# Kernel tuning notes

Hardware: AMD Instinct MI355X
Metric: run time of the kernel (lower is better)

## Reference

```python
import jax, jax.numpy as jnp
import numpy as np

NEG_SLOPE = 0.01  # nn.LeakyReLU default


def setup_inputs() -> dict:
    key = jax.random.key(0)
    k1, k2, k3, k4, k5, k6 = jax.random.split(key, 6)
    N, E, F_IN, F_OUT = 50000, 800000, 256, 64
    x = jax.random.normal(k1, (N, F_IN), dtype=jnp.float32)
    src = jax.random.randint(k2, (E,), 0, N, dtype=jnp.int32)
    dst = jax.random.randint(k3, (E,), 0, N, dtype=jnp.int32)
    # nn.init.normal_(weight, 0, 0.5) for both Linear layers (no bias)
    W1 = 0.5 * jax.random.normal(k4, (F_OUT, F_IN), dtype=jnp.float32)
    W2 = 0.5 * jax.random.normal(k5, (F_OUT, F_OUT), dtype=jnp.float32)
    # detGAT.a = torch.rand(2*out_feats, 1)
    a = jax.random.uniform(k6, (2 * F_OUT, 1), dtype=jnp.float32)
    return {"x": x, "W1": W1, "W2": W2, "a": a, "src": src, "dst": dst}


def reference(x, W1, W2, a, src, dst):
    N, d = x.shape[0], W1.shape[0]
    # model_base: linear -> (dropout, identity in eval) -> relu, twice
    z = jax.nn.relu(x @ W1.T)
    h = jax.nn.relu(z @ W2.T)  # [N, d]
    # detGAT edge score: LeakyReLU(concat([h_dst, h_src]) @ a)
    # split a so we compute per-node dot products once instead of an [E, 2d] concat
    a_dst, a_src = a[:d, 0], a[d:, 0]
    s_dst = h @ a_dst  # [N]
    s_src = h @ a_src  # [N]
    score = jax.nn.leaky_relu(s_dst[dst] + s_src[src], NEG_SLOPE)  # [E]
    # edge_softmax: softmax over incoming edges of each destination node
    m = jax.ops.segment_max(score, dst, num_segments=N)  # [N]
    e = jnp.exp(score - m[dst])
    ssum = jax.ops.segment_sum(e, dst, num_segments=N)  # [N]
    w = e / ssum[dst]  # [E]
    # weighted scatter-sum of src features to dst nodes
    res = jax.ops.segment_sum(h[src] * w[:, None], dst, num_segments=N)  # [N, d]
    return jax.nn.relu(h - res)
```

## Files before the change

### kernel.cpp

```cpp
#include <hip/hip_runtime.h>
#include <math.h>

#define F_IN 256
#define F_OUT 64
#define NEG_SLOPE 0.01f
#define CAP 8192
#define SB 64

typedef unsigned short ushort8_t __attribute__((ext_vector_type(8)));
typedef __bf16 bf16x8 __attribute__((ext_vector_type(8)));
typedef float f32x16 __attribute__((ext_vector_type(16)));

__device__ inline unsigned short f2bf(float f) {
    unsigned u = __float_as_uint(f);
    u += 0x7FFF + ((u >> 16) & 1);
    return (unsigned short)(u >> 16);
}
__device__ inline float bf2f(unsigned short u) {
    return __uint_as_float(((unsigned)u) << 16);
}
__device__ inline void splitbf(float x, unsigned short& hi, unsigned short& lo) {
    hi = f2bf(x);
    lo = f2bf(x - bf2f(hi));
}
__device__ inline bf16x8 asbf8(ushort8_t u) {
    union { ushort8_t u; bf16x8 b; } c; c.u = u; return c.b;
}
__device__ inline float redq32(float v) {
    v += __shfl_xor(v, 1);  v += __shfl_xor(v, 2);  v += __shfl_xor(v, 4);
    v += __shfl_xor(v, 8);  v += __shfl_xor(v, 16);
    return v;
}

__global__ __launch_bounds__(256)
void prep_kernel(const float* __restrict__ W1, const float* __restrict__ W2,
                 unsigned short* __restrict__ w1fh, unsigned short* __restrict__ w1fl,
                 unsigned short* __restrict__ w2fh, unsigned short* __restrict__ w2fl,
                 int* __restrict__ cursor)
{
    int idx = blockIdx.x * 256 + threadIdx.x;
    if (blockIdx.x == 0) cursor[threadIdx.x] = 0;
    int jj = idx & 7, l = (idx >> 3) & 63, t = idx >> 9;
    {
        int nt = t & 1, gks = t >> 1;
        int f = nt * 32 + (l & 31);
        int k = gks * 16 + (l >> 5) * 8 + jj;
        unsigned short hi, lo;
        splitbf(W1[f * F_IN + k], hi, lo);
        w1fh[idx] = hi; w1fl[idx] = lo;
    }
    if (idx < 4096) {
        int nt = t & 1, ks = t >> 1;
        int f = nt * 32 + (l & 31);
        int j = ks * 16 + (l >> 5) * 8 + jj;
        unsigned short hi, lo;
        splitbf(W2[f * F_OUT + j], hi, lo);
        w2fh[idx] = hi; w2fl[idx] = lo;
    }
}

__global__ __launch_bounds__(256, 2)
void mlp_scatter_kernel(const float* __restrict__ x,
                        const unsigned short* __restrict__ w1fh,
                        const unsigned short* __restrict__ w1fl,
                        const unsigned short* __restrict__ w2fh,
                        const unsigned short* __restrict__ w2fl,
                        const float* __restrict__ a,
                        unsigned short* __restrict__ hb,
                        float* __restrict__ sdst,
                        float* __restrict__ ssrc, int N,
                        const int* __restrict__ src, const int* __restrict__ dst,
                        int* __restrict__ cursor, int* __restrict__ edata,
                        int E, int chunk, int MLPB)
{
    __shared__ __align__(16) unsigned short zbuf[4 * 8576];

    const int tid = threadIdx.x;
    const int lane = tid & 63;
    const int bid = blockIdx.x;

    if (bid < MLPB) {
        const int wid = __builtin_amdgcn_readfirstlane(tid >> 6);
        const int ml = lane & 31;
        const int q = lane >> 5;
        const int hl = lane >> 5;
        const int cl = lane & 31;
        const int node0w = bid * 128 + wid * 32;

        unsigned short* xh = zbuf + wid * 8576;
        unsigned short* xl = xh + 4288;
        unsigned short* zh = xh;
        unsigned short* zl = xh + 2112;

        f32x16 acc0, acc1;
#pragma unroll
        for (int i = 0; i < 16; i++) { acc0[i] = 0.f; acc1[i] = 0.f; }

#pragma unroll
        for (int half = 0; half < 2; half++) {
            float4 v[16];
#pragma unroll
            for (int i = 0; i < 16; i++) {
                int r = 2 * i + hl;
                int rr = min(node0w + r, N - 1);
                v[i] = *(const float4*)(x + (size_t)rr * F_IN + half * 128 + cl * 4);
            }
#pragma unroll
            for (int i = 0; i < 16; i++) {
                int r = 2 * i + hl;
                ushort4 h4, l4;
                unsigned short th, tl;
                splitbf(v[i].x, th, tl); h4.x = th; l4.x = tl;
                splitbf(v[i].y, th, tl); h4.y = th; l4.y = tl;
                splitbf(v[i].z, th, tl); h4.z = th; l4.z = tl;
                splitbf(v[i].w, th, tl); h4.w = th; l4.w = tl;
                *(ushort4*)(xh + r * 134 + cl * 4) = h4;
                *(ushort4*)(xl + r * 134 + cl * 4) = l4;
            }
#pragma unroll
            for (int ks = 0; ks < 8; ks++) {
                int gks = half * 8 + ks;
                bf16x8 ah = asbf8(*(const ushort8_t*)(xh + ml * 134 + ks * 16 + q * 8));
                bf16x8 al = asbf8(*(const ushort8_t*)(xl + ml * 134 + ks * 16 + q * 8));
                bf16x8 bh0 = asbf8(*(const ushort8_t*)(w1fh + ((gks * 2 + 0) * 64 + lane) * 8));
                bf16x8 bl0 = asbf8(*(const ushort8_t*)(w1fl + ((gks * 2 + 0) * 64 + lane) * 8));
                bf16x8 bh1 = asbf8(*(const ushort8_t*)(w1fh + ((gks * 2 + 1) * 64 + lane) * 8));
                bf16x8 bl1 = asbf8(*(const ushort8_t*)(w1fl + ((gks * 2 + 1) * 64 + lane) * 8));
                acc0 = __builtin_amdgcn_mfma_f32_32x32x16_bf16(ah, bh0, acc0, 0, 0, 0);
                acc0 = __builtin_amdgcn_mfma_f32_32x32x16_bf16(ah, bl0, acc0, 0, 0, 0);
                acc0 = __builtin_amdgcn_mfma_f32_32x32x16_bf16(al, bh0, acc0, 0, 0, 0);
                acc1 = __builtin_amdgcn_mfma_f32_32x32x16_bf16(ah, bh1, acc1, 0, 0, 0);
                acc1 = __builtin_amdgcn_mfma_f32_32x32x16_bf16(ah, bl1, acc1, 0, 0, 0);
                acc1 = __builtin_amdgcn_mfma_f32_32x32x16_bf16(al, bh1, acc1, 0, 0, 0);
            }
        }

#pragma unroll
        for (int reg = 0; reg < 16; reg++) {
            int nd = (reg & 3) + 8 * (reg >> 2) + 4 * q;
            float z0 = fmaxf(acc0[reg], 0.f);
            float z1 = fmaxf(acc1[reg], 0.f);
            unsigned short h_, l_;
            splitbf(z0, h_, l_);
            zh[nd * 66 + ml] = h_; zl[nd * 66 + ml] = l_;
            splitbf(z1, h_, l_);
            zh[nd * 66 + 32 + ml] = h_; zl[nd * 66 + 32 + ml] = l_;
        }

        f32x16 hacc0, hacc1;
#pragma unroll
        for (int i = 0; i < 16; i++) { hacc0[i] = 0.f; hacc1[i] = 0.f; }
#pragma unroll
        for (int ks = 0; ks < 4; ks++) {
            bf16x8 wh0 = asbf8(*(const ushort8_t*)(w2fh + ((ks * 2 + 0) * 64 + lane) * 8));
            bf16x8 wl0 = asbf8(*(const ushort8_t*)(w2fl + ((ks * 2 + 0) * 64 + lane) * 8));
            bf16x8 wh1 = asbf8(*(const ushort8_t*)(w2fh + ((ks * 2 + 1) * 64 + lane) * 8));
            bf16x8 wl1 = asbf8(*(const ushort8_t*)(w2fl + ((ks * 2 + 1) * 64 + lane) * 8));
            bf16x8 ah = asbf8(*(const ushort8_t*)(zh + ml * 66 + ks * 16 + q * 8));
            bf16x8 al = asbf8(*(const ushort8_t*)(zl + ml * 66 + ks * 16 + q * 8));
            hacc0 = __builtin_amdgcn_mfma_f32_32x32x16_bf16(ah, wh0, hacc0, 0, 0, 0);
            hacc0 = __builtin_amdgcn_mfma_f32_32x32x16_bf16(ah, wl0, hacc0, 0, 0, 0);
            hacc0 = __builtin_amdgcn_mfma_f32_32x32x16_bf16(al, wh0, hacc0, 0, 0, 0);
            hacc1 = __builtin_amdgcn_mfma_f32_32x32x16_bf16(ah, wh1, hacc1, 0, 0, 0);
            hacc1 = __builtin_amdgcn_mfma_f32_32x32x16_bf16(ah, wl1, hacc1, 0, 0, 0);
            hacc1 = __builtin_amdgcn_mfma_f32_32x32x16_bf16(al, wh1, hacc1, 0, 0, 0);
        }

        const float aD0 = a[ml],            aD1 = a[32 + ml];
        const float aS0 = a[F_OUT + ml],    aS1 = a[F_OUT + 32 + ml];

        float sdv = 0.f, ssv = 0.f;
#pragma unroll
        for (int reg = 0; reg < 16; reg++) {
            int nd = (reg & 3) + 8 * (reg >> 2) + 4 * q;
            float h0 = fmaxf(hacc0[reg], 0.f);
            float h1 = fmaxf(hacc1[reg], 0.f);
            float td = redq32(h0 * aD0 + h1 * aD1);
            float ts = redq32(h0 * aS0 + h1 * aS1);
            if (ml == nd) { sdv = td; ssv = ts; }
            int gn = node0w + nd;
            if (gn < N) {
                hb[(size_t)gn * F_OUT + ml]      = f2bf(h0);
                hb[(size_t)gn * F_OUT + 32 + ml] = f2bf(h1);
            }
        }
        {
            int gn = node0w + ml;
            if ((((ml >> 2) & 1) == q) && gn < N) {
                sdst[gn] = sdv;
                ssrc[gn] = ssv;
            }
        }
        return;
    }

    const int sbid = bid - MLPB;
    int* lh = (int*)zbuf;
    int* lbase = lh + 256;
    int* lcur = lh + 512;
    lh[tid] = 0;
    __syncthreads();
    const int beg = sbid * chunk;
    const int end = min(E, beg + chunk);
    for (int i = beg + tid; i < end; i += 256)
        atomicAdd(&lh[((unsigned)dst[i]) >> 8], 1);
    __syncthreads();
    {
        int c = lh[tid];
        lbase[tid] = c ? atomicAdd(&cursor[tid], c) : 0;
        lcur[tid] = 0;
    }
    __syncthreads();
    for (int i = beg + tid; i < end; i += 256) {
        int d = dst[i];
        int s = src[i];
        int b = ((unsigned)d) >> 8;
        int rk = atomicAdd(&lcur[b], 1);
        edata[b * CAP + lbase[b] + rk] = ((d & 0xFF) << 16) | s;
    }
}

__global__ __launch_bounds__(1024)
void sortagg_kernel(const int* __restrict__ cursor,
                    const int* __restrict__ edata,
                    const unsigned short* __restrict__ hb,
                    const float* __restrict__ sdst,
                    const float* __restrict__ ssrc,
                    float* __restrict__ out, int N)
{
    __shared__ int hist[256];
    __shared__ int excl[256];
    __shared__ int start_s[256];
    __shared__ unsigned short ssl[CAP];
    __shared__ float2 ws_sh[16][64];

    const int tid = threadIdx.x;
    const int lane = tid & 63;
    const int wid = tid >> 6;
    const int cb = blockIdx.x;
    const int base = cb * CAP;
    const int ecnt = cursor[cb];

    if (tid < 256) hist[tid] = 0;
    __syncthreads();
    for (int i = tid; i < ecnt; i += 1024)
        atomicAdd(&hist[((unsigned)edata[base + i]) >> 16], 1);
    __syncthreads();

    if (tid < 64) {
        int v0 = hist[lane * 4], v1 = hist[lane * 4 + 1];
        int v2 = hist[lane * 4 + 2], v3 = hist[lane * 4 + 3];
        int ts = v0 + v1 + v2 + v3;
        int s = ts;
#pragma unroll
        for (int d = 1; d < 64; d <<= 1) {
            int t = __shfl_up(s, d);
            if (lane >= d) s += t;
        }
        int e = s - ts;
        excl[lane * 4] = e;
        excl[lane * 4 + 1] = e + v0;
        excl[lane * 4 + 2] = e + v0 + v1;
        excl[lane * 4 + 3] = e + v0 + v1 + v2;
    }
    __syncthreads();
    if (tid < 256) start_s[tid] = excl[tid];
    __syncthreads();

    for (int i = tid; i < ecnt; i += 1024) {
        int pack = edata[base + i];
        int low = ((unsigned)pack) >> 16;
        int rk = atomicAdd(&excl[low], 1);
        ssl[rk] = (unsigned short)(pack & 0xFFFF);
    }
    __syncthreads();

    const int g = lane >> 4;
    const int li = lane & 15;
    const int grp = wid * 4 + g;

    for (int rep = 0; rep < 4; rep++) {
        const int local = rep * 64 + grp;
        const int d = cb * 256 + local;
        const bool vd = d < N;
        const int off = vd ? start_s[local] : 0;
        const int deg = vd ? hist[local] : 0;
        const float sdd = vd ? sdst[d] : 0.f;

        float M = -INFINITY, S = 0.f;
        float c0 = 0.f, c1 = 0.f, c2 = 0.f, c3 = 0.f;

        for (int ch = 0; ch < deg; ch += 16) {
            int ce = min(16, deg - ch);
            float score = -INFINITY;
            int s = 0;
            if (li < ce) {
                s = ssl[off + ch + li];
                float sc = sdd + ssrc[s];
                score = sc > 0.f ? sc : NEG_SLOPE * sc;
            }
            float mc = score;
            mc = fmaxf(mc, __shfl_xor(mc, 1));
            mc = fmaxf(mc, __shfl_xor(mc, 2));
            mc = fmaxf(mc, __shfl_xor(mc, 4));
            mc = fmaxf(mc, __shfl_xor(mc, 8));
            float newM = fmaxf(M, mc);
            float scale = __expf(M - newM);
            float w = (li < ce) ? __expf(score - newM) : 0.f;
            ws_sh[wid][lane] = make_float2(w, __int_as_float(s));
            float csum = w;
            csum += __shfl_xor(csum, 1);
            csum += __shfl_xor(csum, 2);
            csum += __shfl_xor(csum, 4);
            csum += __shfl_xor(csum, 8);
            S = S * scale + csum;
            __builtin_amdgcn_wave_barrier();

            float t0 = 0.f, t1 = 0.f, t2 = 0.f, t3 = 0.f;
#pragma unroll
            for (int e = 0; e < 16; e++) {
                float2 tw = ws_sh[wid][g * 16 + e];
                int se = __float_as_int(tw.y);
                ushort4 r = *(const ushort4*)(hb + (((size_t)(unsigned)se) << 6) + li * 4);
                t0 = fmaf(tw.x, bf2f(r.x), t0);
                t1 = fmaf(tw.x, bf2f(r.y), t1);
                t2 = fmaf(tw.x, bf2f(r.z), t2);
                t3 = fmaf(tw.x, bf2f(r.w), t3);
            }
            c0 = c0 * scale + t0;
            c1 = c1 * scale + t1;
            c2 = c2 * scale + t2;
            c3 = c3 * scale + t3;
            __builtin_amdgcn_wave_barrier();
            M = newM;
        }

        if (vd) {
            ushort4 hr = *(const ushort4*)(hb + (((size_t)(unsigned)d) << 6) + li * 4);
            float inv = (S > 0.f) ? 1.f / S : 0.f;
            float r0 = bf2f(hr.x) - c0 * inv;
            float r1 = bf2f(hr.y) - c1 * inv;
            float r2 = bf2f(hr.z) - c2 * inv;
            float r3 = bf2f(hr.w) - c3 * inv;
            float4 o;
            o.x = r0 > 0.f ? r0 : 0.f;
            o.y = r1 > 0.f ? r1 : 0.f;
            o.z = r2 > 0.f ? r2 : 0.f;
            o.w = r3 > 0.f ? r3 : 0.f;
            *(float4*)(out + (size_t)d * F_OUT + li * 4) = o;
        }
    }
}

extern "C" void kernel_launch(void* const* d_in, const int* in_sizes, int n_in,
                              void* d_out, int out_size, void* d_ws,
                              size_t ws_size, hipStream_t stream)
{
    const float* x  = (const float*)d_in[0];
    const float* W1 = (const float*)d_in[1];
    const float* W2 = (const float*)d_in[2];
    const float* a  = (const float*)d_in[3];
    const int* src  = (const int*)d_in[4];
    const int* dst  = (const int*)d_in[5];
    const int N = in_sizes[0] / F_IN;
    const int E = in_sizes[4];

    float* ws = (float*)d_ws;
    float* sdst = ws;
    float* ssrc = sdst + N;
    unsigned short* w1fh = (unsigned short*)(ssrc + N);
    unsigned short* w1fl = w1fh + 16384;
    unsigned short* w2fh = w1fl + 16384;
    unsigned short* w2fl = w2fh + 4096;
    unsigned short* hb = w2fl + 4096;
    int* cursor = (int*)(hb + (size_t)N * F_OUT);
    int* edata  = cursor + 256;

    const int nbc = (N + 255) >> 8;
    const int MLPB = (N + 127) >> 7;
    const int chunk = (E + SB - 1) / SB;

    prep_kernel<<<64, 256, 0, stream>>>(W1, W2, w1fh, w1fl, w2fh, w2fl, cursor);
    mlp_scatter_kernel<<<MLPB + SB, 256, 0, stream>>>(x, w1fh, w1fl, w2fh, w2fl, a,
                                                      hb, sdst, ssrc, N,
                                                      src, dst, cursor, edata,
                                                      E, chunk, MLPB);
    sortagg_kernel<<<nbc, 1024, 0, stream>>>(cursor, edata, hb, sdst, ssrc,
                                             (float*)d_out, N);
}
```

Before: 147.9 us.

## Software-pipeline x loads in quarter chunks and halve LDS for higher occupancy

Splits the K dimension of the first GEMM into four 64-wide quarters instead of two halves, prefetching the next quarter of x into registers while the current one is split to bf16 and fed to MFMA. This halves the per-wave LDS staging buffer and raises launch bounds from 2 to 4 blocks per SM, aiming to hide global load latency and improve occupancy. The register prefetch plus a tighter register budget may cause spills, and the last iteration issues a redundant reload of quarter 3. The zl region (offset 2112, size up to 2112) still fits within the 4480-element per-wave slot.

Result: slower. 150.8 us (+2.0%).

```diff
diff --git a/kernel.cpp b/kernel.cpp
--- a/kernel.cpp
+++ b/kernel.cpp
@@ -59,7 +59,7 @@
     }
 }
 
-__global__ __launch_bounds__(256, 2)
+__global__ __launch_bounds__(256, 4)
 void mlp_scatter_kernel(const float* __restrict__ x,
                         const unsigned short* __restrict__ w1fh,
                         const unsigned short* __restrict__ w1fl,
@@ -73,7 +73,7 @@
                         int* __restrict__ cursor, int* __restrict__ edata,
                         int E, int chunk, int MLPB)
 {
-    __shared__ __align__(16) unsigned short zbuf[4 * 8576];
+    __shared__ __align__(16) unsigned short zbuf[4 * 4480];
 
     const int tid = threadIdx.x;
     const int lane = tid & 63;
@@ -83,12 +83,12 @@
         const int wid = __builtin_amdgcn_readfirstlane(tid >> 6);
         const int ml = lane & 31;
         const int q = lane >> 5;
-        const int hl = lane >> 5;
-        const int cl = lane & 31;
+        const int rq = lane >> 4;
+        const int cq = lane & 15;
         const int node0w = bid * 128 + wid * 32;
 
-        unsigned short* xh = zbuf + wid * 8576;
-        unsigned short* xl = xh + 4288;
+        unsigned short* xh = zbuf + wid * 4480;
+        unsigned short* xl = xh + 2240;
         unsigned short* zh = xh;
         unsigned short* zl = xh + 2112;
 
@@ -96,32 +96,41 @@
 #pragma unroll
         for (int i = 0; i < 16; i++) { acc0[i] = 0.f; acc1[i] = 0.f; }
 
-#pragma unroll
-        for (int half = 0; half < 2; half++) {
-            float4 v[16];
-#pragma unroll
-            for (int i = 0; i < 16; i++) {
-                int r = 2 * i + hl;
-                int rr = min(node0w + r, N - 1);
-                v[i] = *(const float4*)(x + (size_t)rr * F_IN + half * 128 + cl * 4);
-            }
-#pragma unroll
-            for (int i = 0; i < 16; i++) {
-                int r = 2 * i + hl;
+        int srow[8];
+#pragma unroll
+        for (int i = 0; i < 8; i++)
+            srow[i] = min(node0w + i * 4 + rq, N - 1);
+
+        float4 v[8];
+#pragma unroll
+        for (int i = 0; i < 8; i++)
+            v[i] = *(const float4*)(x + (size_t)srow[i] * F_IN + cq * 4);
+
+#pragma unroll
+        for (int qt = 0; qt < 4; qt++) {
+            const int nqt = qt < 3 ? qt + 1 : 3;
+            float4 vn[8];
+#pragma unroll
+            for (int i = 0; i < 8; i++)
+                vn[i] = *(const float4*)(x + (size_t)srow[i] * F_IN + nqt * 64 + cq * 4);
+
+#pragma unroll
+            for (int i = 0; i < 8; i++) {
+                int r = i * 4 + rq;
                 ushort4 h4, l4;
                 unsigned short th, tl;
                 splitbf(v[i].x, th, tl); h4.x = th; l4.x = tl;
                 splitbf(v[i].y, th, tl); h4.y = th; l4.y = tl;
                 splitbf(v[i].z, th, tl); h4.z = th; l4.z = tl;
                 splitbf(v[i].w, th, tl); h4.w = th; l4.w = tl;
-                *(ushort4*)(xh + r * 134 + cl * 4) = h4;
-                *(ushort4*)(xl + r * 134 + cl * 4) = l4;
-            }
-#pragma unroll
-            for (int ks = 0; ks < 8; ks++) {
-                int gks = half * 8 + ks;
-                bf16x8 ah = asbf8(*(const ushort8_t*)(xh + ml * 134 + ks * 16 + q * 8));
-                bf16x8 al = asbf8(*(const ushort8_t*)(xl + ml * 134 + ks * 16 + q * 8));
+                *(ushort4*)(xh + r * 70 + cq * 4) = h4;
+                *(ushort4*)(xl + r * 70 + cq * 4) = l4;
+            }
+#pragma unroll
+            for (int ks = 0; ks < 4; ks++) {
+                int gks = qt * 4 + ks;
+                bf16x8 ah = asbf8(*(const ushort8_t*)(xh + ml * 70 + ks * 16 + q * 8));
+                bf16x8 al = asbf8(*(const ushort8_t*)(xl + ml * 70 + ks * 16 + q * 8));
                 bf16x8 bh0 = asbf8(*(const ushort8_t*)(w1fh + ((gks * 2 + 0) * 64 + lane) * 8));
                 bf16x8 bl0 = asbf8(*(const ushort8_t*)(w1fl + ((gks * 2 + 0) * 64 + lane) * 8));
                 bf16x8 bh1 = asbf8(*(const ushort8_t*)(w1fh + ((gks * 2 + 1) * 64 + lane) * 8));
@@ -133,6 +142,8 @@
                 acc1 = __builtin_amdgcn_mfma_f32_32x32x16_bf16(ah, bl1, acc1, 0, 0, 0);
                 acc1 = __builtin_amdgcn_mfma_f32_32x32x16_bf16(al, bh1, acc1, 0, 0, 0);
             }
+#pragma unroll
+            for (int i = 0; i < 8; i++) v[i] = vn[i];
         }
 
 #pragma unroll
```

## Stream x tiles via global_load_lds double-buffer and split to bf16 in registers

Applied to the files above, without the earlier changes.

Replaces the load-all-rows-then-convert-to-LDS staging of x with a direct global-to-LDS async copy (global_load_lds) into two per-wave fp32 buffers. These are double-buffered across 8 K-stages with vmcnt waits, and the buffer index is XOR-swizzled to avoid bank conflicts. The hi/lo bf16 split now happens in registers right before the MFMAs, and the smaller LDS footprint allows occupancy to rise to 4 blocks per CU. The intent is to overlap x loads with matrix work and cut register and LDS pressure. The risks are manual vmcnt accounting correctness and redundant split work.

New measurement: 151.4 us. 2.4% more time.

```diff
diff --git a/kernel.cpp b/kernel.cpp
--- a/kernel.cpp
+++ b/kernel.cpp
@@ -26,10 +26,30 @@
 __device__ inline bf16x8 asbf8(ushort8_t u) {
     union { ushort8_t u; bf16x8 b; } c; c.u = u; return c.b;
 }
+__device__ inline void split8(const float4& p0, const float4& p1, bf16x8& ah, bf16x8& al) {
+    ushort8_t h, l;
+    unsigned short th, tl;
+    splitbf(p0.x, th, tl); h[0] = th; l[0] = tl;
+    splitbf(p0.y, th, tl); h[1] = th; l[1] = tl;
+    splitbf(p0.z, th, tl); h[2] = th; l[2] = tl;
+    splitbf(p0.w, th, tl); h[3] = th; l[3] = tl;
+    splitbf(p1.x, th, tl); h[4] = th; l[4] = tl;
+    splitbf(p1.y, th, tl); h[5] = th; l[5] = tl;
+    splitbf(p1.z, th, tl); h[6] = th; l[6] = tl;
+    splitbf(p1.w, th, tl); h[7] = th; l[7] = tl;
+    ah = asbf8(h); al = asbf8(l);
+}
 __device__ inline float redq32(float v) {
     v += __shfl_xor(v, 1);  v += __shfl_xor(v, 2);  v += __shfl_xor(v, 4);
     v += __shfl_xor(v, 8);  v += __shfl_xor(v, 16);
     return v;
+}
+
+__device__ inline void gll16(const void* gsrc, void* lds) {
+    __builtin_amdgcn_global_load_lds(
+        (const __attribute__((address_space(1))) unsigned int*)gsrc,
+        (__attribute__((address_space(3))) unsigned int*)lds,
+        16, 0, 0);
 }
 
 __global__ __launch_bounds__(256)
@@ -59,7 +79,7 @@
     }
 }
 
-__global__ __launch_bounds__(256, 2)
+__global__ __launch_bounds__(256, 4)
 void mlp_scatter_kernel(const float* __restrict__ x,
                         const unsigned short* __restrict__ w1fh,
                         const unsigned short* __restrict__ w1fl,
@@ -73,7 +93,7 @@
                         int* __restrict__ cursor, int* __restrict__ edata,
                         int E, int chunk, int MLPB)
 {
-    __shared__ __align__(16) unsigned short zbuf[4 * 8576];
+    __shared__ __align__(16) unsigned short zbuf[4 * 4224];
 
     const int tid = threadIdx.x;
     const int lane = tid & 63;
@@ -83,45 +103,57 @@
         const int wid = __builtin_amdgcn_readfirstlane(tid >> 6);
         const int ml = lane & 31;
         const int q = lane >> 5;
-        const int hl = lane >> 5;
-        const int cl = lane & 31;
         const int node0w = bid * 128 + wid * 32;
 
-        unsigned short* xh = zbuf + wid * 8576;
-        unsigned short* xl = xh + 4288;
-        unsigned short* zh = xh;
-        unsigned short* zl = xh + 2112;
+        float* bufA = (float*)(zbuf + wid * 4224);
+        float* bufB = (float*)(zbuf + wid * 4224 + 2112);
+        unsigned short* zh = zbuf + wid * 4224;
+        unsigned short* zl = zh + 2112;
+
+        const int rrel_base = lane >> 3;
+        const int slot_w = (lane & 7) >> 1;
+        const int half_w = lane & 1;
 
         f32x16 acc0, acc1;
 #pragma unroll
         for (int i = 0; i < 16; i++) { acc0[i] = 0.f; acc1[i] = 0.f; }
 
-#pragma unroll
-        for (int half = 0; half < 2; half++) {
-            float4 v[16];
-#pragma unroll
-            for (int i = 0; i < 16; i++) {
-                int r = 2 * i + hl;
-                int rr = min(node0w + r, N - 1);
-                v[i] = *(const float4*)(x + (size_t)rr * F_IN + half * 128 + cl * 4);
-            }
-#pragma unroll
-            for (int i = 0; i < 16; i++) {
-                int r = 2 * i + hl;
-                ushort4 h4, l4;
-                unsigned short th, tl;
-                splitbf(v[i].x, th, tl); h4.x = th; l4.x = tl;
-                splitbf(v[i].y, th, tl); h4.y = th; l4.y = tl;
-                splitbf(v[i].z, th, tl); h4.z = th; l4.z = tl;
-                splitbf(v[i].w, th, tl); h4.w = th; l4.w = tl;
-                *(ushort4*)(xh + r * 134 + cl * 4) = h4;
-                *(ushort4*)(xl + r * 134 + cl * 4) = l4;
-            }
-#pragma unroll
-            for (int ks = 0; ks < 8; ks++) {
-                int gks = half * 8 + ks;
-                bf16x8 ah = asbf8(*(const ushort8_t*)(xh + ml * 134 + ks * 16 + q * 8));
-                bf16x8 al = asbf8(*(const ushort8_t*)(xl + ml * 134 + ks * 16 + q * 8));
+        {
+#pragma unroll
+            for (int i = 0; i < 4; i++) {
+                int rrel = i * 8 + rrel_base;
+                int r = min(node0w + rrel, N - 1);
+                int gblk = slot_w ^ (rrel & 3);
+                gll16(x + (size_t)r * F_IN + 0 * 32 + gblk * 8 + half_w * 4,
+                      (char*)bufA + i * 1024);
+            }
+        }
+#pragma unroll
+        for (int st = 0; st < 8; st++) {
+            float* cur = (st & 1) ? bufB : bufA;
+            float* nxt = (st & 1) ? bufA : bufB;
+            if (st < 7) {
+#pragma unroll
+                for (int i = 0; i < 4; i++) {
+                    int rrel = i * 8 + rrel_base;
+                    int r = min(node0w + rrel, N - 1);
+                    int gblk = slot_w ^ (rrel & 3);
+                    gll16(x + (size_t)r * F_IN + (st + 1) * 32 + gblk * 8 + half_w * 4,
+                          (char*)nxt + i * 1024);
+                }
+                asm volatile("s_waitcnt vmcnt(4)" ::: "memory");
+            } else {
+                asm volatile("s_waitcnt vmcnt(0)" ::: "memory");
+            }
+#pragma unroll
+            for (int ks = 0; ks < 2; ks++) {
+                int gks = st * 2 + ks;
+                int sl = (ks * 2 + q) ^ (ml & 3);
+                const float* p = cur + ml * 32 + sl * 8;
+                float4 lo = *(const float4*)p;
+                float4 hi = *(const float4*)(p + 4);
+                bf16x8 ah, al;
+                split8(lo, hi, ah, al);
                 bf16x8 bh0 = asbf8(*(const ushort8_t*)(w1fh + ((gks * 2 + 0) * 64 + lane) * 8));
                 bf16x8 bl0 = asbf8(*(const ushort8_t*)(w1fl + ((gks * 2 + 0) * 64 + lane) * 8));
                 bf16x8 bh1 = asbf8(*(const ushort8_t*)(w1fh + ((gks * 2 + 1) * 64 + lane) * 8));
```

## Move edge scatter into prep kernel with 1024-thread blocks, split MLP kernel

Applied to the files above, without the earlier changes.

The edge bucket-scatter pass leaves the MLP kernel and now runs inside the weight-prep kernel, using 256 blocks of 1024 threads instead of 64 blocks of 256. The MLP runs as its own kernel, and the cursor reset becomes a hipMemsetAsync. The aim is to spread the scatter over more of the GPU and make the MLP kernel simpler. In exchange there is an extra launch plus a memset, and the scatter no longer runs alongside the MLP blocks.

New measurement: 152.8 us. 3.3% more time.

```diff
diff --git a/kernel.cpp b/kernel.cpp
--- a/kernel.cpp
+++ b/kernel.cpp
@@ -5,7 +5,7 @@
 #define F_OUT 64
 #define NEG_SLOPE 0.01f
 #define CAP 8192
-#define SB 64
+#define NB2 256
 
 typedef unsigned short ushort8_t __attribute__((ext_vector_type(8)));
 typedef __bf16 bf16x8 __attribute__((ext_vector_type(8)));
@@ -32,191 +32,187 @@
     return v;
 }
 
-__global__ __launch_bounds__(256)
-void prep_kernel(const float* __restrict__ W1, const float* __restrict__ W2,
-                 unsigned short* __restrict__ w1fh, unsigned short* __restrict__ w1fl,
-                 unsigned short* __restrict__ w2fh, unsigned short* __restrict__ w2fl,
-                 int* __restrict__ cursor)
+__global__ __launch_bounds__(1024)
+void prep_scatter_kernel(const float* __restrict__ W1, const float* __restrict__ W2,
+                         unsigned short* __restrict__ w1fh, unsigned short* __restrict__ w1fl,
+                         unsigned short* __restrict__ w2fh, unsigned short* __restrict__ w2fl,
+                         const int* __restrict__ src, const int* __restrict__ dst,
+                         int* __restrict__ cursor, int* __restrict__ edata,
+                         int E, int chunk)
 {
-    int idx = blockIdx.x * 256 + threadIdx.x;
-    if (blockIdx.x == 0) cursor[threadIdx.x] = 0;
-    int jj = idx & 7, l = (idx >> 3) & 63, t = idx >> 9;
-    {
-        int nt = t & 1, gks = t >> 1;
-        int f = nt * 32 + (l & 31);
-        int k = gks * 16 + (l >> 5) * 8 + jj;
-        unsigned short hi, lo;
-        splitbf(W1[f * F_IN + k], hi, lo);
-        w1fh[idx] = hi; w1fl[idx] = lo;
-    }
-    if (idx < 4096) {
-        int nt = t & 1, ks = t >> 1;
-        int f = nt * 32 + (l & 31);
-        int j = ks * 16 + (l >> 5) * 8 + jj;
-        unsigned short hi, lo;
-        splitbf(W2[f * F_OUT + j], hi, lo);
-        w2fh[idx] = hi; w2fl[idx] = lo;
-    }
-}
-
-__global__ __launch_bounds__(256, 2)
-void mlp_scatter_kernel(const float* __restrict__ x,
-                        const unsigned short* __restrict__ w1fh,
-                        const unsigned short* __restrict__ w1fl,
-                        const unsigned short* __restrict__ w2fh,
-                        const unsigned short* __restrict__ w2fl,
-                        const float* __restrict__ a,
-                        unsigned short* __restrict__ hb,
-                        float* __restrict__ sdst,
-                        float* __restrict__ ssrc, int N,
-                        const int* __restrict__ src, const int* __restrict__ dst,
-                        int* __restrict__ cursor, int* __restrict__ edata,
-                        int E, int chunk, int MLPB)
-{
-    __shared__ __align__(16) unsigned short zbuf[4 * 8576];
-
+    __shared__ int lh[256], lbase[256], lcur[256];
     const int tid = threadIdx.x;
-    const int lane = tid & 63;
-    const int bid = blockIdx.x;
-
-    if (bid < MLPB) {
-        const int wid = __builtin_amdgcn_readfirstlane(tid >> 6);
-        const int ml = lane & 31;
-        const int q = lane >> 5;
-        const int hl = lane >> 5;
-        const int cl = lane & 31;
-        const int node0w = bid * 128 + wid * 32;
-
-        unsigned short* xh = zbuf + wid * 8576;
-        unsigned short* xl = xh + 4288;
-        unsigned short* zh = xh;
-        unsigned short* zl = xh + 2112;
-
-        f32x16 acc0, acc1;
-#pragma unroll
-        for (int i = 0; i < 16; i++) { acc0[i] = 0.f; acc1[i] = 0.f; }
-
-#pragma unroll
-        for (int half = 0; half < 2; half++) {
-            float4 v[16];
-#pragma unroll
-            for (int i = 0; i < 16; i++) {
-                int r = 2 * i + hl;
-                int rr = min(node0w + r, N - 1);
-                v[i] = *(const float4*)(x + (size_t)rr * F_IN + half * 128 + cl * 4);
-            }
-#pragma unroll
-            for (int i = 0; i < 16; i++) {
-                int r = 2 * i + hl;
-                ushort4 h4, l4;
-                unsigned short th, tl;
-                splitbf(v[i].x, th, tl); h4.x = th; l4.x = tl;
-                splitbf(v[i].y, th, tl); h4.y = th; l4.y = tl;
-                splitbf(v[i].z, th, tl); h4.z = th; l4.z = tl;
-                splitbf(v[i].w, th, tl); h4.w = th; l4.w = tl;
-                *(ushort4*)(xh + r * 134 + cl * 4) = h4;
-                *(ushort4*)(xl + r * 134 + cl * 4) = l4;
-            }
-#pragma unroll
-            for (int ks = 0; ks < 8; ks++) {
-                int gks = half * 8 + ks;
-                bf16x8 ah = asbf8(*(const ushort8_t*)(xh + ml * 134 + ks * 16 + q * 8));
-                bf16x8 al = asbf8(*(const ushort8_t*)(xl + ml * 134 + ks * 16 + q * 8));
-                bf16x8 bh0 = asbf8(*(const ushort8_t*)(w1fh + ((gks * 2 + 0) * 64 + lane) * 8));
-                bf16x8 bl0 = asbf8(*(const ushort8_t*)(w1fl + ((gks * 2 + 0) * 64 + lane) * 8));
-                bf16x8 bh1 = asbf8(*(const ushort8_t*)(w1fh + ((gks * 2 + 1) * 64 + lane) * 8));
-                bf16x8 bl1 = asbf8(*(const ushort8_t*)(w1fl + ((gks * 2 + 1) * 64 + lane) * 8));
-                acc0 = __builtin_amdgcn_mfma_f32_32x32x16_bf16(ah, bh0, acc0, 0, 0, 0);
-                acc0 = __builtin_amdgcn_mfma_f32_32x32x16_bf16(ah, bl0, acc0, 0, 0, 0);
-                acc0 = __builtin_amdgcn_mfma_f32_32x32x16_bf16(al, bh0, acc0, 0, 0, 0);
-                acc1 = __builtin_amdgcn_mfma_f32_32x32x16_bf16(ah, bh1, acc1, 0, 0, 0);
-                acc1 = __builtin_amdgcn_mfma_f32_32x32x16_bf16(ah, bl1, acc1, 0, 0, 0);
-                acc1 = __builtin_amdgcn_mfma_f32_32x32x16_bf16(al, bh1, acc1, 0, 0, 0);
-            }
-        }
-
-#pragma unroll
-        for (int reg = 0; reg < 16; reg++) {
-            int nd = (reg & 3) + 8 * (reg >> 2) + 4 * q;
-            float z0 = fmaxf(acc0[reg], 0.f);
-            float z1 = fmaxf(acc1[reg], 0.f);
-            unsigned short h_, l_;
-            splitbf(z0, h_, l_);
-            zh[nd * 66 + ml] = h_; zl[nd * 66 + ml] = l_;
-            splitbf(z1, h_, l_);
-            zh[nd * 66 + 32 + ml] = h_; zl[nd * 66 + 32 + ml] = l_;
-        }
-
-        f32x16 hacc0, hacc1;
-#pragma unroll
-        for (int i = 0; i < 16; i++) { hacc0[i] = 0.f; hacc1[i] = 0.f; }
-#pragma unroll
-        for (int ks = 0; ks < 4; ks++) {
-            bf16x8 wh0 = asbf8(*(const ushort8_t*)(w2fh + ((ks * 2 + 0) * 64 + lane) * 8));
-            bf16x8 wl0 = asbf8(*(const ushort8_t*)(w2fl + ((ks * 2 + 0) * 64 + lane) * 8));
-            bf16x8 wh1 = asbf8(*(const ushort8_t*)(w2fh + ((ks * 2 + 1) * 64 + lane) * 8));
-            bf16x8 wl1 = asbf8(*(const ushort8_t*)(w2fl + ((ks * 2 + 1) * 64 + lane) * 8));
-            bf16x8 ah = asbf8(*(const ushort8_t*)(zh + ml * 66 + ks * 16 + q * 8));
-            bf16x8 al = asbf8(*(const ushort8_t*)(zl + ml * 66 + ks * 16 + q * 8));
-            hacc0 = __builtin_amdgcn_mfma_f32_32x32x16_bf16(ah, wh0, hacc0, 0, 0, 0);
-            hacc0 = __builtin_amdgcn_mfma_f32_32x32x16_bf16(ah, wl0, hacc0, 0, 0, 0);
-            hacc0 = __builtin_amdgcn_mfma_f32_32x32x16_bf16(al, wh0, hacc0, 0, 0, 0);
-            hacc1 = __builtin_amdgcn_mfma_f32_32x32x16_bf16(ah, wh1, hacc1, 0, 0, 0);
-            hacc1 = __builtin_amdgcn_mfma_f32_32x32x16_bf16(ah, wl1, hacc1, 0, 0, 0);
-            hacc1 = __builtin_amdgcn_mfma_f32_32x32x16_bf16(al, wh1, hacc1, 0, 0, 0);
-        }
-
-        const float aD0 = a[ml],            aD1 = a[32 + ml];
-        const float aS0 = a[F_OUT + ml],    aS1 = a[F_OUT + 32 + ml];
-
-        float sdv = 0.f, ssv = 0.f;
-#pragma unroll
-        for (int reg = 0; reg < 16; reg++) {
-            int nd = (reg & 3) + 8 * (reg >> 2) + 4 * q;
-            float h0 = fmaxf(hacc0[reg], 0.f);
-            float h1 = fmaxf(hacc1[reg], 0.f);
-            float td = redq32(h0 * aD0 + h1 * aD1);
-            float ts = redq32(h0 * aS0 + h1 * aS1);
-            if (ml == nd) { sdv = td; ssv = ts; }
-            int gn = node0w + nd;
-            if (gn < N) {
-                hb[(size_t)gn * F_OUT + ml]      = f2bf(h0);
-                hb[(size_t)gn * F_OUT + 32 + ml] = f2bf(h1);
-            }
-        }
+
+    if (blockIdx.x < 16) {
+        int idx = blockIdx.x * 1024 + tid;
+        int jj = idx & 7, l = (idx >> 3) & 63, t = idx >> 9;
         {
-            int gn = node0w + ml;
-            if ((((ml >> 2) & 1) == q) && gn < N) {
-                sdst[gn] = sdv;
-                ssrc[gn] = ssv;
-            }
+            int nt = t & 1, gks = t >> 1;
+            int f = nt * 32 + (l & 31);
+            int k = gks * 16 + (l >> 5) * 8 + jj;
+            unsigned short hi, lo;
+            splitbf(W1[f * F_IN + k], hi, lo);
+            w1fh[idx] = hi; w1fl[idx] = lo;
+        }
+        if (idx < 4096) {
+            int nt = t & 1, ks = t >> 1;
+            int f = nt * 32 + (l & 31);
+            int j = ks * 16 + (l >> 5) * 8 + jj;
+            unsigned short hi, lo;
+            splitbf(W2[f * F_OUT + j], hi, lo);
+            w2fh[idx] = hi; w2fl[idx] = lo;
         }
         return;
     }
 
-    const int sbid = bid - MLPB;
-    int* lh = (int*)zbuf;
-    int* lbase = lh + 256;
-    int* lcur = lh + 512;
-    lh[tid] = 0;
-    __syncthreads();
-    const int beg = sbid * chunk;
+    const int bid = blockIdx.x - 16;
+    if (tid < 256) lh[tid] = 0;
+    __syncthreads();
+    const int beg = bid * chunk;
     const int end = min(E, beg + chunk);
-    for (int i = beg + tid; i < end; i += 256)
+    for (int i = beg + tid; i < end; i += 1024)
         atomicAdd(&lh[((unsigned)dst[i]) >> 8], 1);
     __syncthreads();
-    {
+    if (tid < 256) {
         int c = lh[tid];
         lbase[tid] = c ? atomicAdd(&cursor[tid], c) : 0;
         lcur[tid] = 0;
     }
     __syncthreads();
-    for (int i = beg + tid; i < end; i += 256) {
+    for (int i = beg + tid; i < end; i += 1024) {
         int d = dst[i];
         int s = src[i];
         int b = ((unsigned)d) >> 8;
         int rk = atomicAdd(&lcur[b], 1);
         edata[b * CAP + lbase[b] + rk] = ((d & 0xFF) << 16) | s;
+    }
+}
+
+__global__ __launch_bounds__(256, 2)
+void mlp_kernel(const float* __restrict__ x,
+                const unsigned short* __restrict__ w1fh,
+                const unsigned short* __restrict__ w1fl,
+                const unsigned short* __restrict__ w2fh,
+                const unsigned short* __restrict__ w2fl,
+                const float* __restrict__ a,
+                unsigned short* __restrict__ hb,
+                float* __restrict__ sdst,
+                float* __restrict__ ssrc, int N)
+{
+    __shared__ __align__(16) unsigned short zbuf[4 * 8576];
+
+    const int tid = threadIdx.x;
+    const int lane = tid & 63;
+    const int wid = __builtin_amdgcn_readfirstlane(tid >> 6);
+    const int ml = lane & 31;
+    const int q = lane >> 5;
+    const int hl = lane >> 5;
+    const int cl = lane & 31;
+    const int node0w = blockIdx.x * 128 + wid * 32;
+
+    unsigned short* xh = zbuf + wid * 8576;
+    unsigned short* xl = xh + 4288;
+    unsigned short* zh = xh;
+    unsigned short* zl = xh + 2112;
+
+    f32x16 acc0, acc1;
+#pragma unroll
+    for (int i = 0; i < 16; i++) { acc0[i] = 0.f; acc1[i] = 0.f; }
+
+#pragma unroll
+    for (int half = 0; half < 2; half++) {
+        float4 v[16];
+#pragma unroll
+        for (int i = 0; i < 16; i++) {
+            int r = 2 * i + hl;
+            int rr = min(node0w + r, N - 1);
+            v[i] = *(const float4*)(x + (size_t)rr * F_IN + half * 128 + cl * 4);
+        }
+#pragma unroll
+        for (int i = 0; i < 16; i++) {
+            int r = 2 * i + hl;
+            ushort4 h4, l4;
+            unsigned short th, tl;
+            splitbf(v[i].x, th, tl); h4.x = th; l4.x = tl;
+            splitbf(v[i].y, th, tl); h4.y = th; l4.y = tl;
+            splitbf(v[i].z, th, tl); h4.z = th; l4.z = tl;
+            splitbf(v[i].w, th, tl); h4.w = th; l4.w = tl;
+            *(ushort4*)(xh + r * 134 + cl * 4) = h4;
+            *(ushort4*)(xl + r * 134 + cl * 4) = l4;
+        }
+#pragma unroll
+        for (int ks = 0; ks < 8; ks++) {
+            int gks = half * 8 + ks;
+            bf16x8 ah = asbf8(*(const ushort8_t*)(xh + ml * 134 + ks * 16 + q * 8));
+            bf16x8 al = asbf8(*(const ushort8_t*)(xl + ml * 134 + ks * 16 + q * 8));
+            bf16x8 bh0 = asbf8(*(const ushort8_t*)(w1fh + ((gks * 2 + 0) * 64 + lane) * 8));
+            bf16x8 bl0 = asbf8(*(const ushort8_t*)(w1fl + ((gks * 2 + 0) * 64 + lane) * 8));
+            bf16x8 bh1 = asbf8(*(const ushort8_t*)(w1fh + ((gks * 2 + 1) * 64 + lane) * 8));
+            bf16x8 bl1 = asbf8(*(const ushort8_t*)(w1fl + ((gks * 2 + 1) * 64 + lane) * 8));
+            acc0 = __builtin_amdgcn_mfma_f32_32x32x16_bf16(ah, bh0, acc0, 0, 0, 0);
+            acc0 = __builtin_amdgcn_mfma_f32_32x32x16_bf16(ah, bl0, acc0, 0, 0, 0);
+            acc0 = __builtin_amdgcn_mfma_f32_32x32x16_bf16(al, bh0, acc0, 0, 0, 0);
+            acc1 = __builtin_amdgcn_mfma_f32_32x32x16_bf16(ah, bh1, acc1, 0, 0, 0);
+            acc1 = __builtin_amdgcn_mfma_f32_32x32x16_bf16(ah, bl1, acc1, 0, 0, 0);
+            acc1 = __builtin_amdgcn_mfma_f32_32x32x16_bf16(al, bh1, acc1, 0, 0, 0);
+        }
+    }
+
+#pragma unroll
+    for (int reg = 0; reg < 16; reg++) {
+        int nd = (reg & 3) + 8 * (reg >> 2) + 4 * q;
+        float z0 = fmaxf(acc0[reg], 0.f);
+        float z1 = fmaxf(acc1[reg], 0.f);
+        unsigned short h_, l_;
+        splitbf(z0, h_, l_);
+        zh[nd * 66 + ml] = h_; zl[nd * 66 + ml] = l_;
+        splitbf(z1, h_, l_);
+        zh[nd * 66 + 32 + ml] = h_; zl[nd * 66 + 32 + ml] = l_;
+    }
+
+    f32x16 hacc0, hacc1;
+#pragma unroll
+    for (int i = 0; i < 16; i++) { hacc0[i] = 0.f; hacc1[i] = 0.f; }
+#pragma unroll
+    for (int ks = 0; ks < 4; ks++) {
+        bf16x8 wh0 = asbf8(*(const ushort8_t*)(w2fh + ((ks * 2 + 0) * 64 + lane) * 8));
+        bf16x8 wl0 = asbf8(*(const ushort8_t*)(w2fl + ((ks * 2 + 0) * 64 + lane) * 8));
+        bf16x8 wh1 = asbf8(*(const ushort8_t*)(w2fh + ((ks * 2 + 1) * 64 + lane) * 8));
+        bf16x8 wl1 = asbf8(*(const ushort8_t*)(w2fl + ((ks * 2 + 1) * 64 + lane) * 8));
+        bf16x8 ah = asbf8(*(const ushort8_t*)(zh + ml * 66 + ks * 16 + q * 8));
+        bf16x8 al = asbf8(*(const ushort8_t*)(zl + ml * 66 + ks * 16 + q * 8));
+        hacc0 = __builtin_amdgcn_mfma_f32_32x32x16_bf16(ah, wh0, hacc0, 0, 0, 0);
+        hacc0 = __builtin_amdgcn_mfma_f32_32x32x16_bf16(ah, wl0, hacc0, 0, 0, 0);
+        hacc0 = __builtin_amdgcn_mfma_f32_32x32x16_bf16(al, wh0, hacc0, 0, 0, 0);
+        hacc1 = __builtin_amdgcn_mfma_f32_32x32x16_bf16(ah, wh1, hacc1, 0, 0, 0);
+        hacc1 = __builtin_amdgcn_mfma_f32_32x32x16_bf16(ah, wl1, hacc1, 0, 0, 0);
+        hacc1 = __builtin_amdgcn_mfma_f32_32x32x16_bf16(al, wh1, hacc1, 0, 0, 0);
+    }
+
+    const float aD0 = a[ml],            aD1 = a[32 + ml];
+    const float aS0 = a[F_OUT + ml],    aS1 = a[F_OUT + 32 + ml];
+
+    float sdv = 0.f, ssv = 0.f;
+#pragma unroll
+    for (int reg = 0; reg < 16; reg++) {
+        int nd = (reg & 3) + 8 * (reg >> 2) + 4 * q;
+        float h0 = fmaxf(hacc0[reg], 0.f);
+        float h1 = fmaxf(hacc1[reg], 0.f);
+        float td = redq32(h0 * aD0 + h1 * aD1);
+        float ts = redq32(h0 * aS0 + h1 * aS1);
+        if (ml == nd) { sdv = td; ssv = ts; }
+        int gn = node0w + nd;
+        if (gn < N) {
+            hb[(size_t)gn * F_OUT + ml]      = f2bf(h0);
+            hb[(size_t)gn * F_OUT + 32 + ml] = f2bf(h1);
+        }
+    }
+    {
+        int gn = node0w + ml;
+        if ((((ml >> 2) & 1) == q) && gn < N) {
+            sdst[gn] = sdv;
+            ssrc[gn] = ssv;
+        }
     }
 }
 
@@ -378,13 +374,13 @@
 
     const int nbc = (N + 255) >> 8;
     const int MLPB = (N + 127) >> 7;
-    const int chunk = (E + SB - 1) / SB;
-
-    prep_kernel<<<64, 256, 0, stream>>>(W1, W2, w1fh, w1fl, w2fh, w2fl, cursor);
-    mlp_scatter_kernel<<<MLPB + SB, 256, 0, stream>>>(x, w1fh, w1fl, w2fh, w2fl, a,
-                                                      hb, sdst, ssrc, N,
-                                                      src, dst, cursor, edata,
-                                                      E, chunk, MLPB);
+    const int chunk = (E + NB2 - 1) / NB2;
+
+    hipMemsetAsync(cursor, 0, 256 * sizeof(int), stream);
+    prep_scatter_kernel<<<16 + NB2, 1024, 0, stream>>>(W1, W2, w1fh, w1fl, w2fh, w2fl,
+                                                       src, dst, cursor, edata, E, chunk);
+    mlp_kernel<<<MLPB, 256, 0, stream>>>(x, w1fh, w1fl, w2fh, w2fl, a,
+                                         hb, sdst, ssrc, N);
     sortagg_kernel<<<nbc, 1024, 0, stream>>>(cursor, edata, hb, sdst, ssrc,
                                              (float*)d_out, N);
 }
```
